# Kernel tuning notes

Measured on AMD Instinct MI355X. Metric: run time of the kernel, lower is better.

## Reference

```python
import jax, jax.numpy as jnp
import numpy as np

L = 28          # layers
D = 1024        # hidden
HQ = 16         # query heads
HKV = 8         # kv heads
HD = 128        # head dim
DFF = 3072      # mlp intermediate
Q = 512         # prefill length (= end_step, past_kv_len = 0)
EPS = 1e-6


def setup_inputs() -> dict:
    key = jax.random.key(0)
    ks = jax.random.split(key, 12)
    s = 0.02
    hidden_states = jax.random.normal(ks[0], (1, Q, D), jnp.float32)
    # RoPE tables (concatenated-halves layout, base 1e6 as in Qwen3)
    pos = jnp.arange(Q, dtype=jnp.float32)
    inv_freq = 1.0 / (1e6 ** (jnp.arange(0, HD, 2, dtype=jnp.float32) / HD))
    freqs = pos[:, None] * inv_freq[None, :]              # [Q, HD/2]
    emb = jnp.concatenate([freqs, freqs], axis=-1)        # [Q, HD]
    position_cos = jnp.cos(emb)[None]                     # [1, Q, HD]
    position_sin = jnp.sin(emb)[None]
    # causal mask: 0 where key_pos <= query_pos else -1e9 ; [1,1,Q,Q]
    i = jnp.arange(Q)
    attention_mask = jnp.where(i[None, :] <= i[:, None], 0.0, -1e9).astype(jnp.float32)[None, None]
    # stacked per-layer weights (torch Linear y = x @ W^T stored here as [in,out])
    Wq = jax.random.normal(ks[1], (L, D, HQ * HD), jnp.float32) * s
    Wk = jax.random.normal(ks[2], (L, D, HKV * HD), jnp.float32) * s
    Wv = jax.random.normal(ks[3], (L, D, HKV * HD), jnp.float32) * s
    Wo = jax.random.normal(ks[4], (L, HQ * HD, D), jnp.float32) * s
    Wg = jax.random.normal(ks[5], (L, D, DFF), jnp.float32) * s
    Wu = jax.random.normal(ks[6], (L, D, DFF), jnp.float32) * s
    Wd = jax.random.normal(ks[7], (L, DFF, D), jnp.float32) * s
    ln1 = jnp.ones((L, D), jnp.float32)
    ln2 = jnp.ones((L, D), jnp.float32)
    qn = jnp.ones((L, HD), jnp.float32)
    kn = jnp.ones((L, HD), jnp.float32)
    return {"hidden_states": hidden_states, "position_cos": position_cos,
            "position_sin": position_sin, "attention_mask": attention_mask,
            "Wq": Wq, "Wk": Wk, "Wv": Wv, "Wo": Wo, "Wg": Wg, "Wu": Wu, "Wd": Wd,
            "ln1": ln1, "ln2": ln2, "qn": qn, "kn": kn}


def rmsnorm(x, w):
    return x * jax.lax.rsqrt(jnp.mean(x * x, axis=-1, keepdims=True) + EPS) * w


def rotate_half(x):
    x1, x2 = jnp.split(x, 2, axis=-1)
    return jnp.concatenate([-x2, x1], axis=-1)


def reference(hidden_states, position_cos, position_sin, attention_mask,
              Wq, Wk, Wv, Wo, Wg, Wu, Wd, ln1, ln2, qn, kn):
    q_len = hidden_states.shape[1]
    scale = 1.0 / np.sqrt(HD)
    cos = position_cos[:, None]   # [1,1,Q,HD] broadcast over heads
    sin = position_sin[:, None]

    def layer(h, p):
        wq, wk, wv, wo, wg, wu, wd, l1, l2, qw, kw = p
        x = rmsnorm(h, l1)
        q = (x @ wq).reshape(1, q_len, HQ, HD).transpose(0, 2, 1, 3)   # [1,HQ,Q,HD]
        k = (x @ wk).reshape(1, q_len, HKV, HD).transpose(0, 2, 1, 3)  # [1,HKV,Q,HD]
        v = (x @ wv).reshape(1, q_len, HKV, HD).transpose(0, 2, 1, 3)
        q = rmsnorm(q, qw)
        k = rmsnorm(k, kw)
        q = q * cos + rotate_half(q) * sin
        k = k * cos + rotate_half(k) * sin
        # fp16 KV-cache round trip (faithful to k.half() store / .float() load)
        k = k.astype(jnp.float16).astype(jnp.float32)
        v = v.astype(jnp.float16).astype(jnp.float32)
        # GQA: repeat kv heads
        k = jnp.repeat(k, HQ // HKV, axis=1)
        v = jnp.repeat(v, HQ // HKV, axis=1)
        scores = jnp.einsum('bhqd,bhkd->bhqk', q, k) * scale + attention_mask
        probs = jax.nn.softmax(scores, axis=-1)
        attn = jnp.einsum('bhqk,bhkd->bhqd', probs, v)
        attn = attn.transpose(0, 2, 1, 3).reshape(1, q_len, HQ * HD)
        h = h + attn @ wo
        y = rmsnorm(h, l2)
        h = h + (jax.nn.silu(y @ wg) * (y @ wu)) @ wd
        return h, None

    params = (Wq, Wk, Wv, Wo, Wg, Wu, Wd, ln1, ln2, qn, kn)
    out, _ = jax.lax.scan(layer, hidden_states, params)
    return out
```

## Files before the change

kernel.cpp:

```cpp
#include <hip/hip_runtime.h>
#include <stdint.h>


typedef __bf16 bf16_t;
typedef _Float16 f16_t;
typedef __bf16 bf16x8 __attribute__((ext_vector_type(8)));
typedef __bf16 bf16x4 __attribute__((ext_vector_type(4)));
typedef _Float16 f16x8 __attribute__((ext_vector_type(8)));
typedef float f32x4 __attribute__((ext_vector_type(4)));

#define SEQ 512
#define NHQ 16
#define NHKV 8
#define HD 128

#define IMG_QKV 0ull
#define IMG_WO  8388608ull
#define IMG_GU  12582912ull
#define IMG_WD  25165824ull
#define IMG_LAYER_BYTES 31457280ull

typedef const __attribute__((address_space(1))) uint32_t as1_u32;
typedef __attribute__((address_space(3))) uint32_t as3_u32;

__device__ __forceinline__ void gload16(const void* g, void* l) {
    __builtin_amdgcn_global_load_lds((as1_u32*)g, (as3_u32*)l, 16, 0, 0);
}

#define WAITV6 asm volatile("s_waitcnt vmcnt(6)" ::: "memory")
#define WAITV0 asm volatile("s_waitcnt vmcnt(0)" ::: "memory")

__device__ __forceinline__ size_t aoff(int row, int col, int ldak) {
    return (((size_t)((row >> 6) * ldak + (col >> 6))) << 13) +
           ((size_t)(row & 63) << 7) +
           (size_t)((((col & 63) << 1)) ^ ((row & 7) << 4));
}

__global__ __launch_bounds__(256) void k_copy(const float* __restrict__ src,
                                              float* __restrict__ dst)
{
    size_t i = ((size_t)blockIdx.x * 256 + threadIdx.x) * 4;
    *(float4*)(dst + i) = *(const float4*)(src + i);
}

__device__ __forceinline__ void conv_tile(
    int b, int lay,
    const float* __restrict__ Wq, const float* __restrict__ Wk,
    const float* __restrict__ Wv, const float* __restrict__ Wo,
    const float* __restrict__ Wg, const float* __restrict__ Wu,
    const float* __restrict__ Wd, char* __restrict__ ib, void* smemv)
{
    const float* wq = Wq + (size_t)lay * 1024 * 2048;
    const float* wk = Wk + (size_t)lay * 1024 * 1024;
    const float* wv = Wv + (size_t)lay * 1024 * 1024;
    const float* wo = Wo + (size_t)lay * 2048 * 1024;
    const float* wg = Wg + (size_t)lay * 1024 * 3072;
    const float* wu = Wu + (size_t)lay * 1024 * 3072;
    const float* wd = Wd + (size_t)lay * 3072 * 1024;

    const float* src = nullptr;
    int ldbw = 0, n, kt, guMode = 0;
    size_t dstoff;
    if (b < 1024) {
        n = b >> 4; kt = b & 15;
        int C0 = n * 64;
        if (C0 < 2048)      { src = wq + C0;          ldbw = 2048; }
        else if (C0 < 3072) { src = wk + (C0 - 2048); ldbw = 1024; }
        else                { src = wv + (C0 - 3072); ldbw = 1024; }
        src += (size_t)(kt * 64) * ldbw;
        dstoff = IMG_QKV + (size_t)b * 8192;
    } else if (b < 1536) {
        int b2 = b - 1024; n = b2 >> 5; kt = b2 & 31;
        src = wo + (size_t)(kt * 64) * 1024 + n * 64; ldbw = 1024;
        dstoff = IMG_WO + (size_t)b2 * 8192;
    } else if (b < 3072) {
        int b3 = b - 1536; n = b3 >> 4; kt = b3 & 15;
        guMode = 1; ldbw = 3072;
        dstoff = IMG_GU + (size_t)b3 * 8192;
    } else {
        int b4 = b - 3072; n = b4 / 48; kt = b4 % 48;
        src = wd + (size_t)(kt * 64) * 1024 + n * 64; ldbw = 1024;
        dstoff = IMG_WD + (size_t)b4 * 8192;
    }

    float (*T)[68] = (float (*)[68])smemv;
    int tid = threadIdx.x;
    if (!guMode) {
#pragma unroll
        for (int it = 0; it < 4; ++it) {
            int idx = it * 256 + tid;
            int kk = idx >> 4, seg = idx & 15;
            *(float4*)&T[kk][seg * 4] = *(const float4*)(src + (size_t)kk * ldbw + seg * 4);
        }
    } else {
        const float* wg_ = wg + (size_t)(kt * 64) * 3072;
        const float* wu_ = wu + (size_t)(kt * 64) * 3072;
#pragma unroll
        for (int it = 0; it < 4; ++it) {
            int idx = it * 256 + tid;
            int kk = idx >> 4, seg = idx & 15;
            int nl = seg * 4;
            int colc = n * 32 + ((nl >> 5) & 1) * 16 + (nl & 15);
            const float* s2 = (((nl >> 4) & 1) ? wu_ : wg_) + (size_t)kk * 3072 + colc;
            *(float4*)&T[kk][nl] = *(const float4*)s2;
        }
    }
    __syncthreads();
    char* dst = ib + dstoff;
#pragma unroll
    for (int it = 0; it < 2; ++it) {
        int kg = tid & 7;
        int nrow = it * 32 + (tid >> 3);
        bf16x8 o;
#pragma unroll
        for (int j = 0; j < 8; ++j) o[j] = (bf16_t)T[kg * 8 + j][nrow];
        *(bf16x8*)(dst + nrow * 128 + ((kg * 16) ^ ((nrow & 7) << 4))) = o;
    }
}

__global__ __launch_bounds__(256) void k_conv(
    int lay,
    const float* __restrict__ Wq, const float* __restrict__ Wk,
    const float* __restrict__ Wv, const float* __restrict__ Wo,
    const float* __restrict__ Wg, const float* __restrict__ Wu,
    const float* __restrict__ Wd, char* __restrict__ img)
{
    __shared__ __align__(16) char smem[17408];
    conv_tile(blockIdx.x, lay, Wq, Wk, Wv, Wo, Wg, Wu, Wd, img, smem);
}

__global__ __launch_bounds__(256) void k_rms(
    float* __restrict__ h, const bf16_t* __restrict__ parts, int nparts,
    const float* __restrict__ w, char* __restrict__ ximg)
{
    int t = blockIdx.x, tid = threadIdx.x;
    size_t base = (size_t)t * 1024 + tid * 4;
    float4 v = *(const float4*)(h + base);
    for (int p = 0; p < nparts; ++p) {
        bf16x4 a = *(const bf16x4*)(parts + (size_t)p * 524288 + base);
        v.x += (float)a[0]; v.y += (float)a[1]; v.z += (float)a[2]; v.w += (float)a[3];
    }
    if (nparts) *(float4*)(h + base) = v;
    float ss = v.x * v.x + v.y * v.y + v.z * v.z + v.w * v.w;
#pragma unroll
    for (int m = 1; m < 64; m <<= 1) ss += __shfl_xor(ss, m);
    __shared__ float red[4];
    if ((tid & 63) == 0) red[tid >> 6] = ss;
    __syncthreads();
    float tot = (red[0] + red[1]) + (red[2] + red[3]);
    float sc = rsqrtf(tot * (1.0f / 1024.0f) + 1e-6f);
    float4 wv4 = *(const float4*)(w + tid * 4);
    bf16x4 o;
    o[0] = (bf16_t)(v.x * sc * wv4.x);
    o[1] = (bf16_t)(v.y * sc * wv4.y);
    o[2] = (bf16_t)(v.z * sc * wv4.z);
    o[3] = (bf16_t)(v.w * sc * wv4.w);
    *(bf16x4*)(ximg + aoff(t, tid * 4, 16)) = o;
}

__global__ __launch_bounds__(256) void k_finalize(
    const float* __restrict__ h, const bf16_t* __restrict__ parts,
    float* __restrict__ out)
{
    size_t base = ((size_t)blockIdx.x * 256 + threadIdx.x) * 4;
    float4 v = *(const float4*)(h + base);
#pragma unroll
    for (int p = 0; p < 4; ++p) {
        bf16x4 a = *(const bf16x4*)(parts + (size_t)p * 524288 + base);
        v.x += (float)a[0]; v.y += (float)a[1]; v.z += (float)a[2]; v.w += (float)a[3];
    }
    *(float4*)(out + base) = v;
}

template <int NBN, int SPLITK, int LDAK>
__device__ __forceinline__ void gemm_loop(
    const char* __restrict__ Aimg, const char* __restrict__ Bimg,
    char* smem, int f, f32x4 (&acc)[2][4], int& bmO, int& bnO, int& sO)
{
    const int steps = LDAK / SPLITK;
    int bm = f / (NBN * SPLITK);
    int r = f % (NBN * SPLITK);
    int s = r / NBN;
    int bn = r % NBN;
    int k0d = s * steps;
    bmO = bm; bnO = bn; sO = s;

    int tid = threadIdx.x;
    int wv = tid >> 6, l = tid & 63, lg = l >> 4, lr = l & 15;
    int wr = wv >> 1, wc = wv & 1;

#pragma unroll
    for (int i = 0; i < 2; ++i)
#pragma unroll
        for (int j = 0; j < 4; ++j) { f32x4 z = {0.f, 0.f, 0.f, 0.f}; acc[i][j] = z; }

    auto stage = [&](int buf, int kt) {
        const char* ab = Aimg + ((size_t)(bm * LDAK + k0d + kt)) * 8192;
        const char* b0 = Bimg + ((size_t)((2 * bn) * LDAK + k0d + kt)) * 8192;
        const char* b1 = Bimg + ((size_t)((2 * bn + 1) * LDAK + k0d + kt)) * 8192;
        char* al = smem + buf * 24576;
        char* bl = al + 8192;
#pragma unroll
        for (int u = 0; u < 2; ++u) {
            int off = (wv * 2 + u) * 1024;
            gload16(ab + off + l * 16, al + off);
        }
#pragma unroll
        for (int u = 0; u < 4; ++u) {
            int off = (wv * 4 + u) * 1024;
            const char* src = (off < 8192) ? (b0 + off) : (b1 + off - 8192);
            gload16(src + l * 16, bl + off);
        }
    };
    auto compute = [&](int buf) {
        const char* as = smem + buf * 24576;
        const char* bs = as + 8192 + wc * 8192;
        __builtin_amdgcn_s_setprio(1);
#pragma unroll
        for (int c = 0; c < 2; ++c) {
            int co = (c * 64 + lg * 16) ^ ((lr & 7) << 4);
            bf16x8 af[2], bf[4];
#pragma unroll
            for (int i = 0; i < 2; ++i)
                af[i] = *(const bf16x8*)(as + (wr * 32 + i * 16 + lr) * 128 + co);
#pragma unroll
            for (int j = 0; j < 4; ++j)
                bf[j] = *(const bf16x8*)(bs + (j * 16 + lr) * 128 + co);
#pragma unroll
            for (int i = 0; i < 2; ++i)
#pragma unroll
                for (int j = 0; j < 4; ++j)
                    acc[i][j] = __builtin_amdgcn_mfma_f32_16x16x32_bf16(
                        af[i], bf[j], acc[i][j], 0, 0, 0);
        }
        __builtin_amdgcn_s_setprio(0);
    };

    stage(0, 0);
    int buf = 0;
    for (int kt = 0; kt < steps; ++kt) {
        if (kt + 1 < steps) { stage(buf ^ 1, kt + 1); WAITV6; }
        else                { WAITV0; }
        __builtin_amdgcn_sched_barrier(0);
        __builtin_amdgcn_s_barrier();
        __builtin_amdgcn_sched_barrier(0);
        compute(buf);
        __builtin_amdgcn_s_barrier();
        buf ^= 1;
    }
}

__global__ __launch_bounds__(256) void g_qkvf(
    const char* __restrict__ Aimg, const char* __restrict__ Bimg,
    const float* __restrict__ cosb, const float* __restrict__ sinb,
    const float* __restrict__ qw, const float* __restrict__ kw,
    f16_t* __restrict__ qf, f16_t* __restrict__ kf, f16_t* __restrict__ vT)
{
    __shared__ __align__(128) char smem[49152];
    f32x4 acc[2][4];
    int bm, bn, s;
    gemm_loop<32, 1, 16>(Aimg, Bimg, smem, blockIdx.x, acc, bm, bn, s);

    int tid = threadIdx.x;
    int wv = tid >> 6, l = tid & 63, lg = l >> 4, lr = l & 15;
    int wr = wv >> 1, wc = wv & 1;
    float (*X)[132] = (float (*)[132])smem;
#pragma unroll
    for (int i = 0; i < 2; ++i)
#pragma unroll
        for (int j = 0; j < 4; ++j)
#pragma unroll
            for (int ii = 0; ii < 4; ++ii)
                X[wr * 32 + i * 16 + lg * 4 + ii][wc * 64 + j * 16 + lr] = acc[i][j][ii];
    __syncthreads();

    int t0 = bm * 64;
    if (bn < 24) {
        bool isq = bn < 16;
        int slot = isq ? bn : bn - 16;
        const float* wn = isq ? qw : kw;
        int r = tid >> 2, part = tid & 3;
        float ss = 0.f;
#pragma unroll
        for (int c = 0; c < 32; ++c) { float v = X[r][part * 32 + c]; ss += v * v; }
        ss += __shfl_xor(ss, 1);
        ss += __shfl_xor(ss, 2);
        float sc = rsqrtf(ss * (1.0f / 128.0f) + 1e-6f);
        int t = t0 + r;
        int d0 = part * 16;
        float o1v[16], o2v[16];
#pragma unroll
        for (int c = 0; c < 16; ++c) {
            int d = d0 + c;
            float xv1 = X[r][d] * sc * wn[d];
            float xv2 = X[r][d + 64] * sc * wn[d + 64];
            o1v[c] = xv1 * cosb[t * HD + d] - xv2 * sinb[t * HD + d];
            o2v[c] = xv2 * cosb[t * HD + d + 64] + xv1 * sinb[t * HD + d + 64];
        }
        f16x8 w0, w1, w2, w3;
#pragma unroll
        for (int c = 0; c < 8; ++c) {
            w0[c] = (f16_t)o1v[c];     w1[c] = (f16_t)o1v[8 + c];
            w2[c] = (f16_t)o2v[c];     w3[c] = (f16_t)o2v[8 + c];
        }
        f16_t* o = (isq ? qf : kf) + ((size_t)slot * SEQ + t) * HD;
        *(f16x8*)(o + d0) = w0;
        *(f16x8*)(o + d0 + 8) = w1;
        *(f16x8*)(o + d0 + 64) = w2;
        *(f16x8*)(o + d0 + 72) = w3;
    } else {
        int kvh = bn - 24;
#pragma unroll
        for (int it = 0; it < 4; ++it) {
            int task = it * 256 + tid;
            int d = task >> 3, seg = task & 7;
            f16x8 o;
#pragma unroll
            for (int j = 0; j < 8; ++j) o[j] = (f16_t)X[seg * 8 + j][d];
            *(f16x8*)(vT + ((size_t)kvh * HD + d) * SEQ + t0 + seg * 8) = o;
        }
    }
}

__global__ __launch_bounds__(256) void g_wo(const char* A, const char* B, bf16_t* parts)
{
    __shared__ __align__(128) char smem[49152];
    f32x4 acc[2][4];
    int bm, bn, s;
    gemm_loop<8, 4, 32>(A, B, smem, blockIdx.x, acc, bm, bn, s);
    int tid = threadIdx.x;
    int wv = tid >> 6, l = tid & 63, lg = l >> 4, lr = l & 15;
    int wr = wv >> 1, wc = wv & 1;
    bf16_t* P = parts + (size_t)s * 524288;
#pragma unroll
    for (int i = 0; i < 2; ++i)
#pragma unroll
        for (int j = 0; j < 4; ++j)
#pragma unroll
            for (int ii = 0; ii < 4; ++ii) {
                int row = bm * 64 + wr * 32 + i * 16 + lg * 4 + ii;
                int col = bn * 128 + wc * 64 + j * 16 + lr;
                P[(size_t)row * 1024 + col] = (bf16_t)acc[i][j][ii];
            }
}

__device__ __forceinline__ void wd_gemm(const char* A, const char* B,
                                        bf16_t* parts, char* smem, int f)
{
    f32x4 acc[2][4];
    int bm, bn, s;
    gemm_loop<8, 4, 48>(A, B, smem, f, acc, bm, bn, s);
    int tid = threadIdx.x;
    int wv = tid >> 6, l = tid & 63, lg = l >> 4, lr = l & 15;
    int wr = wv >> 1, wc = wv & 1;
    bf16_t* P = parts + (size_t)s * 524288;
#pragma unroll
    for (int i = 0; i < 2; ++i)
#pragma unroll
        for (int j = 0; j < 4; ++j)
#pragma unroll
            for (int ii = 0; ii < 4; ++ii) {
                int row = bm * 64 + wr * 32 + i * 16 + lg * 4 + ii;
                int col = bn * 128 + wc * 64 + j * 16 + lr;
                P[(size_t)row * 1024 + col] = (bf16_t)acc[i][j][ii];
            }
}

__global__ __launch_bounds__(256) void g_gu(const char* A, const char* B, char* mimg)
{
    __shared__ __align__(128) char smem[49152];
    f32x4 acc[2][4];
    int bm, bn, s;
    gemm_loop<48, 1, 16>(A, B, smem, blockIdx.x, acc, bm, bn, s);
    int tid = threadIdx.x;
    int wv = tid >> 6, l = tid & 63, lg = l >> 4, lr = l & 15;
    int wr = wv >> 1, wc = wv & 1;
#pragma unroll
    for (int i = 0; i < 2; ++i)
#pragma unroll
        for (int jp = 0; jp < 2; ++jp)
#pragma unroll
            for (int ii = 0; ii < 4; ++ii) {
                int row = bm * 64 + wr * 32 + i * 16 + lg * 4 + ii;
                int col = (bn * 2 + wc) * 32 + jp * 16 + lr;
                float gv = acc[i][2 * jp][ii];
                float uv = acc[i][2 * jp + 1][ii];
                float val = gv / (1.f + __expf(-gv)) * uv;
                *(bf16_t*)(mimg + aoff(row, col, 48)) = (bf16_t)val;
            }
}

__global__ __launch_bounds__(256) void k_wdc(
    const char* A, const char* B, bf16_t* parts,
    const float* Wq, const float* Wk, const float* Wv, const float* Wo,
    const float* Wg, const float* Wu, const float* Wd,
    int lnext, char* imgnext)
{
    __shared__ __align__(128) char smem[49152];
    int b = blockIdx.x;
    if (b < 256) wd_gemm(A, B, parts, smem, b);
    else conv_tile(b - 256, lnext, Wq, Wk, Wv, Wo, Wg, Wu, Wd, imgnext, smem);
}

__global__ __launch_bounds__(128) void k_attn(
    const f16_t* __restrict__ qf, const f16_t* __restrict__ kf,
    const f16_t* __restrict__ vT, char* __restrict__ attimg)
{
    int h = blockIdx.x >> 4, qb = blockIdx.x & 15;
    int kvh = h >> 1;
    __shared__ f16_t Kt[64][136];
    __shared__ f16_t Vt[128][72];
    __shared__ f16_t Pl[2][16][72];
    int tid = threadIdx.x;
    int wv = tid >> 6, l = tid & 63, lg = l >> 4, lr = l & 15;
    int q0 = qb * 32;
    int qrow = q0 + wv * 16;

    f16x8 aq[4];
    const f16_t* qp = qf + ((size_t)h * SEQ + qrow + lr) * HD;
#pragma unroll
    for (int c = 0; c < 4; ++c) aq[c] = *(const f16x8*)(qp + c * 32 + lg * 8);

    f32x4 accv[8];
#pragma unroll
    for (int df = 0; df < 8; ++df) { f32x4 z = {0.f, 0.f, 0.f, 0.f}; accv[df] = z; }
    float mrun[4], lrun[4];
#pragma unroll
    for (int ii = 0; ii < 4; ++ii) { mrun[ii] = -3e38f; lrun[ii] = 0.f; }

    int ktiles = (q0 + 32 + 63) >> 6;
    for (int kt = 0; kt < ktiles; ++kt) {
        int kt0 = kt * 64;
        __syncthreads();
#pragma unroll
        for (int it = 0; it < 8; ++it) {
            int idx = it * 128 + tid;
            int r = idx >> 4, seg = idx & 15;
            *(int4*)&Kt[r][seg * 8] =
                *(const int4*)(kf + ((size_t)kvh * SEQ + kt0 + r) * HD + seg * 8);
        }
#pragma unroll
        for (int it = 0; it < 8; ++it) {
            int idx = it * 128 + tid;
            int r = idx >> 3, seg = idx & 7;
            *(int4*)&Vt[r][seg * 8] =
                *(const int4*)(vT + ((size_t)kvh * HD + r) * SEQ + kt0 + seg * 8);
        }
        __syncthreads();

        f32x4 s[4];
#pragma unroll
        for (int nf = 0; nf < 4; ++nf) {
            f32x4 a = {0.f, 0.f, 0.f, 0.f};
#pragma unroll
            for (int c = 0; c < 4; ++c) {
                f16x8 bk = *(const f16x8*)&Kt[nf * 16 + lr][c * 32 + lg * 8];
                a = __builtin_amdgcn_mfma_f32_16x16x32_f16(aq[c], bk, a, 0, 0, 0);
            }
            s[nf] = a;
        }
        const float scale = 0.08838834764831845f;
        float tmax[4] = {-3e38f, -3e38f, -3e38f, -3e38f};
#pragma unroll
        for (int nf = 0; nf < 4; ++nf) {
            int ktg = kt0 + nf * 16 + lr;
#pragma unroll
            for (int ii = 0; ii < 4; ++ii) {
                int qg = qrow + lg * 4 + ii;
                float vv = s[nf][ii] * scale;
                vv = (ktg <= qg) ? vv : -1e30f;
                s[nf][ii] = vv;
                tmax[ii] = fmaxf(tmax[ii], vv);
            }
        }
#pragma unroll
        for (int m = 1; m < 16; m <<= 1)
#pragma unroll
            for (int ii = 0; ii < 4; ++ii)
                tmax[ii] = fmaxf(tmax[ii], __shfl_xor(tmax[ii], m));
        float corr[4];
#pragma unroll
        for (int ii = 0; ii < 4; ++ii) {
            float mnew = fmaxf(mrun[ii], tmax[ii]);
            corr[ii] = __expf(mrun[ii] - mnew);
            mrun[ii] = mnew;
        }
        float tsum[4] = {0.f, 0.f, 0.f, 0.f};
#pragma unroll
        for (int nf = 0; nf < 4; ++nf)
#pragma unroll
            for (int ii = 0; ii < 4; ++ii) {
                float pp = __expf(s[nf][ii] - mrun[ii]);
                s[nf][ii] = pp;
                tsum[ii] += pp;
            }
#pragma unroll
        for (int m = 1; m < 16; m <<= 1)
#pragma unroll
            for (int ii = 0; ii < 4; ++ii) tsum[ii] += __shfl_xor(tsum[ii], m);
#pragma unroll
        for (int ii = 0; ii < 4; ++ii) lrun[ii] = lrun[ii] * corr[ii] + tsum[ii];
#pragma unroll
        for (int df = 0; df < 8; ++df)
#pragma unroll
            for (int ii = 0; ii < 4; ++ii) accv[df][ii] *= corr[ii];
#pragma unroll
        for (int nf = 0; nf < 4; ++nf)
#pragma unroll
            for (int ii = 0; ii < 4; ++ii)
                Pl[wv][lg * 4 + ii][nf * 16 + lr] = (f16_t)s[nf][ii];
        __syncthreads();
#pragma unroll
        for (int c = 0; c < 2; ++c) {
            f16x8 ap = *(const f16x8*)&Pl[wv][lr][c * 32 + lg * 8];
#pragma unroll
            for (int df = 0; df < 8; ++df) {
                f16x8 bv = *(const f16x8*)&Vt[df * 16 + lr][c * 32 + lg * 8];
                accv[df] = __builtin_amdgcn_mfma_f32_16x16x32_f16(ap, bv, accv[df], 0, 0, 0);
            }
        }
    }
#pragma unroll
    for (int df = 0; df < 8; ++df)
#pragma unroll
        for (int ii = 0; ii < 4; ++ii) {
            int qg = qrow + lg * 4 + ii;
            int col = h * HD + df * 16 + lr;
            *(bf16_t*)(attimg + aoff(qg, col, 32)) =
                (bf16_t)(accv[df][ii] / lrun[ii]);
        }
}

extern "C" void kernel_launch(void* const* d_in, const int* in_sizes, int n_in,
                              void* d_out, int out_size, void* d_ws, size_t ws_size,
                              hipStream_t stream)
{
    const float* hin  = (const float*)d_in[0];
    const float* cosb = (const float*)d_in[1];
    const float* sinb = (const float*)d_in[2];
    const float* Wq = (const float*)d_in[4];
    const float* Wk = (const float*)d_in[5];
    const float* Wv = (const float*)d_in[6];
    const float* Wo = (const float*)d_in[7];
    const float* Wg = (const float*)d_in[8];
    const float* Wu = (const float*)d_in[9];
    const float* Wd = (const float*)d_in[10];
    const float* Ln1 = (const float*)d_in[11];
    const float* Ln2 = (const float*)d_in[12];
    const float* Qn = (const float*)d_in[13];
    const float* Kn = (const float*)d_in[14];

    char* p = (char*)d_ws;
    auto alloc = [&](size_t bytes) { char* r = p; p += bytes; return r; };
    float*  h     = (float*)alloc(2097152);
    bf16_t* parts = (bf16_t*)alloc(4194304);
    char*   ximg  = alloc(1048576);
    char*   yimg  = alloc(1048576);
    char*   attimg= alloc(2097152);
    char*   mimg  = alloc(3145728);
    f16_t*  qf    = (f16_t*)alloc(2097152);
    f16_t*  kf    = (f16_t*)alloc(1048576);
    f16_t*  vT    = (f16_t*)alloc(1048576);
    char*   imgA  = alloc(IMG_LAYER_BYTES);
    size_t fixed = (size_t)(imgA + IMG_LAYER_BYTES - (char*)d_ws);
    bool pp = ws_size >= fixed + IMG_LAYER_BYTES;
    char* imgB = pp ? alloc(IMG_LAYER_BYTES) : imgA;

    k_copy<<<512, 256, 0, stream>>>(hin, h);
    k_conv<<<3840, 256, 0, stream>>>(0, Wq, Wk, Wv, Wo, Wg, Wu, Wd, imgA);

    for (int l = 0; l < 28; ++l) {
        char* img  = (l & 1) ? imgB : imgA;
        char* imgn = (l & 1) ? imgA : imgB;

        k_rms<<<512, 256, 0, stream>>>(h, parts, l == 0 ? 0 : 4,
                                       Ln1 + (size_t)l * 1024, ximg);
        g_qkvf<<<256, 256, 0, stream>>>(ximg, img + IMG_QKV, cosb, sinb,
                                        Qn + (size_t)l * 128, Kn + (size_t)l * 128,
                                        qf, kf, vT);
        k_attn<<<256, 128, 0, stream>>>(qf, kf, vT, attimg);
        g_wo<<<256, 256, 0, stream>>>(attimg, img + IMG_WO, parts);
        k_rms<<<512, 256, 0, stream>>>(h, parts, 4, Ln2 + (size_t)l * 1024, yimg);
        g_gu<<<384, 256, 0, stream>>>(yimg, img + IMG_GU, mimg);

        bool fuse = pp && (l < 27);
        k_wdc<<<fuse ? 4096 : 256, 256, 0, stream>>>(
            mimg, img + IMG_WD, parts, Wq, Wk, Wv, Wo, Wg, Wu, Wd,
            l + 1, imgn);
        if (!pp && l < 27)
            k_conv<<<3840, 256, 0, stream>>>(l + 1, Wq, Wk, Wv, Wo, Wg, Wu, Wd, imgA);
    }
    k_finalize<<<512, 256, 0, stream>>>(h, parts, (float*)d_out);
}
```

Measured before the change: 2.354 ms.

## Spread next-layer weight conversion across four GEMM kernels and reverse attention block order

```diff
diff --git a/kernel.cpp b/kernel.cpp
--- a/kernel.cpp
+++ b/kernel.cpp
@@ -254,9 +254,16 @@
     const char* __restrict__ Aimg, const char* __restrict__ Bimg,
     const float* __restrict__ cosb, const float* __restrict__ sinb,
     const float* __restrict__ qw, const float* __restrict__ kw,
-    f16_t* __restrict__ qf, f16_t* __restrict__ kf, f16_t* __restrict__ vT)
+    f16_t* __restrict__ qf, f16_t* __restrict__ kf, f16_t* __restrict__ vT,
+    const float* Wq, const float* Wk, const float* Wv, const float* Wo,
+    const float* Wg, const float* Wu, const float* Wd,
+    int lnext, char* __restrict__ imgnext)
 {
     __shared__ __align__(128) char smem[49152];
+    if (blockIdx.x >= 256) {
+        conv_tile(blockIdx.x - 256, lnext, Wq, Wk, Wv, Wo, Wg, Wu, Wd, imgnext, smem);
+        return;
+    }
     f32x4 acc[2][4];
     int bm, bn, s;
     gemm_loop<32, 1, 16>(Aimg, Bimg, smem, blockIdx.x, acc, bm, bn, s);
@@ -322,9 +329,17 @@
     }
 }
 
-__global__ __launch_bounds__(256) void g_wo(const char* A, const char* B, bf16_t* parts)
+__global__ __launch_bounds__(256) void g_wo(
+    const char* A, const char* B, bf16_t* parts,
+    const float* Wq, const float* Wk, const float* Wv, const float* Wo,
+    const float* Wg, const float* Wu, const float* Wd,
+    int lnext, char* imgnext)
 {
     __shared__ __align__(128) char smem[49152];
+    if (blockIdx.x >= 256) {
+        conv_tile(blockIdx.x - 256 + 960, lnext, Wq, Wk, Wv, Wo, Wg, Wu, Wd, imgnext, smem);
+        return;
+    }
     f32x4 acc[2][4];
     int bm, bn, s;
     gemm_loop<8, 4, 32>(A, B, smem, blockIdx.x, acc, bm, bn, s);
@@ -344,31 +359,17 @@
             }
 }
 
-__device__ __forceinline__ void wd_gemm(const char* A, const char* B,
-                                        bf16_t* parts, char* smem, int f)
-{
-    f32x4 acc[2][4];
-    int bm, bn, s;
-    gemm_loop<8, 4, 48>(A, B, smem, f, acc, bm, bn, s);
-    int tid = threadIdx.x;
-    int wv = tid >> 6, l = tid & 63, lg = l >> 4, lr = l & 15;
-    int wr = wv >> 1, wc = wv & 1;
-    bf16_t* P = parts + (size_t)s * 524288;
-#pragma unroll
-    for (int i = 0; i < 2; ++i)
-#pragma unroll
-        for (int j = 0; j < 4; ++j)
-#pragma unroll
-            for (int ii = 0; ii < 4; ++ii) {
-                int row = bm * 64 + wr * 32 + i * 16 + lg * 4 + ii;
-                int col = bn * 128 + wc * 64 + j * 16 + lr;
-                P[(size_t)row * 1024 + col] = (bf16_t)acc[i][j][ii];
-            }
-}
-
-__global__ __launch_bounds__(256) void g_gu(const char* A, const char* B, char* mimg)
+__global__ __launch_bounds__(256) void g_gu(
+    const char* A, const char* B, char* mimg,
+    const float* Wq, const float* Wk, const float* Wv, const float* Wo,
+    const float* Wg, const float* Wu, const float* Wd,
+    int lnext, char* imgnext)
 {
     __shared__ __align__(128) char smem[49152];
+    if (blockIdx.x >= 384) {
+        conv_tile(blockIdx.x - 384 + 1920, lnext, Wq, Wk, Wv, Wo, Wg, Wu, Wd, imgnext, smem);
+        return;
+    }
     f32x4 acc[2][4];
     int bm, bn, s;
     gemm_loop<48, 1, 16>(A, B, smem, blockIdx.x, acc, bm, bn, s);
@@ -398,15 +399,34 @@
 {
     __shared__ __align__(128) char smem[49152];
     int b = blockIdx.x;
-    if (b < 256) wd_gemm(A, B, parts, smem, b);
-    else conv_tile(b - 256, lnext, Wq, Wk, Wv, Wo, Wg, Wu, Wd, imgnext, smem);
+    if (b >= 256) {
+        conv_tile(b - 256 + 2880, lnext, Wq, Wk, Wv, Wo, Wg, Wu, Wd, imgnext, smem);
+        return;
+    }
+    f32x4 acc[2][4];
+    int bm, bn, s;
+    gemm_loop<8, 4, 48>(A, B, smem, b, acc, bm, bn, s);
+    int tid = threadIdx.x;
+    int wv = tid >> 6, l = tid & 63, lg = l >> 4, lr = l & 15;
+    int wr = wv >> 1, wc = wv & 1;
+    bf16_t* P = parts + (size_t)s * 524288;
+#pragma unroll
+    for (int i = 0; i < 2; ++i)
+#pragma unroll
+        for (int j = 0; j < 4; ++j)
+#pragma unroll
+            for (int ii = 0; ii < 4; ++ii) {
+                int row = bm * 64 + wr * 32 + i * 16 + lg * 4 + ii;
+                int col = bn * 128 + wc * 64 + j * 16 + lr;
+                P[(size_t)row * 1024 + col] = (bf16_t)acc[i][j][ii];
+            }
 }
 
 __global__ __launch_bounds__(128) void k_attn(
     const f16_t* __restrict__ qf, const f16_t* __restrict__ kf,
     const f16_t* __restrict__ vT, char* __restrict__ attimg)
 {
-    int h = blockIdx.x >> 4, qb = blockIdx.x & 15;
+    int h = blockIdx.x >> 4, qb = 15 - (blockIdx.x & 15);
     int kvh = h >> 1;
     __shared__ f16_t Kt[64][136];
     __shared__ f16_t Vt[128][72];
@@ -572,23 +592,28 @@
     for (int l = 0; l < 28; ++l) {
         char* img  = (l & 1) ? imgB : imgA;
         char* imgn = (l & 1) ? imgA : imgB;
+        bool cv = pp && (l < 27);
+        int ln = l + 1;
 
         k_rms<<<512, 256, 0, stream>>>(h, parts, l == 0 ? 0 : 4,
                                        Ln1 + (size_t)l * 1024, ximg);
-        g_qkvf<<<256, 256, 0, stream>>>(ximg, img + IMG_QKV, cosb, sinb,
-                                        Qn + (size_t)l * 128, Kn + (size_t)l * 128,
-                                        qf, kf, vT);
+        g_qkvf<<<cv ? 1216 : 256, 256, 0, stream>>>(
+            ximg, img + IMG_QKV, cosb, sinb,
+            Qn + (size_t)l * 128, Kn + (size_t)l * 128, qf, kf, vT,
+            Wq, Wk, Wv, Wo, Wg, Wu, Wd, ln, imgn);
         k_attn<<<256, 128, 0, stream>>>(qf, kf, vT, attimg);
-        g_wo<<<256, 256, 0, stream>>>(attimg, img + IMG_WO, parts);
+        g_wo<<<cv ? 1216 : 256, 256, 0, stream>>>(
+            attimg, img + IMG_WO, parts,
+            Wq, Wk, Wv, Wo, Wg, Wu, Wd, ln, imgn);
         k_rms<<<512, 256, 0, stream>>>(h, parts, 4, Ln2 + (size_t)l * 1024, yimg);
-        g_gu<<<384, 256, 0, stream>>>(yimg, img + IMG_GU, mimg);
-
-        bool fuse = pp && (l < 27);
-        k_wdc<<<fuse ? 4096 : 256, 256, 0, stream>>>(
-            mimg, img + IMG_WD, parts, Wq, Wk, Wv, Wo, Wg, Wu, Wd,
-            l + 1, imgn);
+        g_gu<<<cv ? 1536 : 384, 256, 0, stream>>>(
+            yimg, img + IMG_GU, mimg,
+            Wq, Wk, Wv, Wo, Wg, Wu, Wd, ln, imgn);
+        k_wdc<<<cv ? 1216 : 256, 256, 0, stream>>>(
+            mimg, img + IMG_WD, parts,
+            Wq, Wk, Wv, Wo, Wg, Wu, Wd, ln, imgn);
         if (!pp && l < 27)
-            k_conv<<<3840, 256, 0, stream>>>(l + 1, Wq, Wk, Wv, Wo, Wg, Wu, Wd, imgA);
+            k_conv<<<3840, 256, 0, stream>>>(ln, Wq, Wk, Wv, Wo, Wg, Wu, Wd, imgA);
     }
     k_finalize<<<512, 256, 0, stream>>>(h, parts, (float*)d_out);
 }
```

Result: no change. 2.331 ms (median of 2 runs) (-1.0%).
